# Kernel optimization log

Measured on AMD Instinct MI355X. Metric: run time of the kernel, lower is better.

Reference implementation:

```python
import jax, jax.numpy as jnp
import numpy as np

K = 20                      # kNN size (init kwarg k)
_BN_S = 1.0 / np.sqrt(1.0 + 1e-5)  # BatchNorm eval with running var=1, mean=0


def _edge_conv(f, W1, b1, g, be, W2, b2):
    # f: [B,N,C]. DynamicEdgeConv: kNN in feature space (self included, as in
    # torch_cluster.knn), message = MLP([x_i, x_j - x_i]), max aggregation.
    sq = jnp.sum(f * f, -1)
    d = sq[:, :, None] + sq[:, None, :] - 2.0 * jnp.einsum('bnc,bmc->bnm', f, f)
    _, idx = jax.lax.top_k(-d, K)                      # [B,N,K]
    fj = jax.vmap(lambda fb, ib: fb[ib])(f, idx)       # [B,N,K,C] neighbor gather
    fi = jnp.broadcast_to(f[:, :, None, :], fj.shape)
    msg = jnp.concatenate([fi, fj - fi], -1)           # [B,N,K,2C]
    h = jax.nn.relu((msg @ W1 + b1) * (g * _BN_S) + be)  # Linear -> BN(eval) -> ReLU
    h = h @ W2 + b2                                    # plain last MLP layer
    return jnp.max(h, axis=2)                          # max over K neighbors


def _forward(x, pos,
             c1_W1, c1_b1, c1_g, c1_be, c1_W2, c1_b2,
             c2_W1, c2_b1, c2_g, c2_be, c2_W2, c2_b2,
             c3_W1, c3_b1, c3_g, c3_be, c3_W2, c3_b2,
             m_W1, m_b1, m_W2, m_b2, m_W3, m_b3, m_W4, m_b4):
    x0 = jnp.concatenate([x, pos], -1)                 # [B,N,6]
    x1 = _edge_conv(x0, c1_W1, c1_b1, c1_g, c1_be, c1_W2, c1_b2)
    x2 = _edge_conv(x1, c2_W1, c2_b1, c2_g, c2_be, c2_W2, c2_b2)
    x3 = _edge_conv(x2, c3_W1, c3_b1, c3_g, c3_be, c3_W2, c3_b2)
    h = jnp.concatenate([x1, x2, x3], -1)              # [B,N,192]
    # head MLP: norm=None, dropout inactive at inference, plain last layer
    h = jax.nn.relu(h @ m_W1 + m_b1)
    h = jax.nn.relu(h @ m_W2 + m_b2)
    h = jax.nn.relu(h @ m_W3 + m_b3)
    out = h @ m_W4 + m_b4                              # [B,N,40]
    return jax.nn.log_softmax(out, -1)


def setup_inputs() -> dict:
    key = jax.random.key(0)
    ks = iter(jax.random.split(key, 40))

    def lin(cin, cout):
        W = jax.random.normal(next(ks), (cin, cout), jnp.float32) / np.sqrt(cin)
        b = jnp.zeros((cout,), jnp.float32)
        return W, b

    inp = {}
    inp['x'] = jax.random.normal(next(ks), (8, 4096, 3), jnp.float32)
    inp['pos'] = jax.random.normal(next(ks), (8, 4096, 3), jnp.float32)
    for i, cin in zip((1, 2, 3), (12, 128, 128)):      # 2*in_channels of each conv
        W1, b1 = lin(cin, 64)
        W2, b2 = lin(64, 64)
        inp[f'c{i}_W1'], inp[f'c{i}_b1'] = W1, b1
        inp[f'c{i}_g'] = jnp.ones((64,), jnp.float32)
        inp[f'c{i}_be'] = jnp.zeros((64,), jnp.float32)
        inp[f'c{i}_W2'], inp[f'c{i}_b2'] = W2, b2
    dims = [192, 1024, 256, 128, 40]
    for j in range(4):
        W, b = lin(dims[j], dims[j + 1])
        inp[f'm_W{j + 1}'], inp[f'm_b{j + 1}'] = W, b
    return inp


def reference(x, pos,
              c1_W1, c1_b1, c1_g, c1_be, c1_W2, c1_b2,
              c2_W1, c2_b1, c2_g, c2_be, c2_W2, c2_b2,
              c3_W1, c3_b1, c3_g, c3_be, c3_W2, c3_b2,
              m_W1, m_b1, m_W2, m_b2, m_W3, m_b3, m_W4, m_b4):
    return _forward(x, pos,
                    c1_W1, c1_b1, c1_g, c1_be, c1_W2, c1_b2,
                    c2_W1, c2_b1, c2_g, c2_be, c2_W2, c2_b2,
                    c3_W1, c3_b1, c3_g, c3_be, c3_W2, c3_b2,
                    m_W1, m_b1, m_W2, m_b2, m_W3, m_b3, m_W4, m_b4)
```

## Files before the change

kernel.cpp:

```cpp
#include <hip/hip_runtime.h>
#include <math.h>

#define KNN 20
#define NPTS 4096
#define NB 8

__device__ __forceinline__ bool lexless(float d1, int i1, float d2, int i2) {
    return d1 < d2 || (d1 == d2 && i1 < i2);
}

__global__ __launch_bounds__(256) void concat_norm_kernel(const float* __restrict__ x,
                                                          const float* __restrict__ pos,
                                                          float* __restrict__ f0,
                                                          float* __restrict__ nrm, int total) {
    int p = blockIdx.x * 256 + threadIdx.x;
    if (p < total) {
        float v0 = x[(size_t)p*3 + 0], v1 = x[(size_t)p*3 + 1], v2 = x[(size_t)p*3 + 2];
        float v3 = pos[(size_t)p*3 + 0], v4 = pos[(size_t)p*3 + 1], v5 = pos[(size_t)p*3 + 2];
        f0[(size_t)p*6 + 0] = v0; f0[(size_t)p*6 + 1] = v1; f0[(size_t)p*6 + 2] = v2;
        f0[(size_t)p*6 + 3] = v3; f0[(size_t)p*6 + 4] = v4; f0[(size_t)p*6 + 5] = v5;
        float s = 0.f;
        s = fmaf(v0, v0, s); s = fmaf(v1, v1, s); s = fmaf(v2, v2, s);
        s = fmaf(v3, v3, s); s = fmaf(v4, v4, s); s = fmaf(v5, v5, s);
        nrm[p] = s;
    }
}

template<int C>
__global__ __launch_bounds__(256) void norm_kernel(const float* __restrict__ f, int ldf,
                                                   float* __restrict__ norms, int total) {
    int p = blockIdx.x * 256 + threadIdx.x;
    if (p >= total) return;
    const float* fp = f + (size_t)p * ldf;
    float s = 0.f;
    if constexpr ((C & 3) == 0) {
#pragma unroll
        for (int k = 0; k < C; k += 4) {
            float4 v = *(const float4*)(fp + k);
            s = fmaf(v.x, v.x, s); s = fmaf(v.y, v.y, s);
            s = fmaf(v.z, v.z, s); s = fmaf(v.w, v.w, s);
        }
    } else {
#pragma unroll
        for (int k = 0; k < C; ++k) s = fmaf(fp[k], fp[k], s);
    }
    norms[p] = s;
}

#define KCHAIN(ck_) do {                                                 \
    unsigned long long kc = (ck_);                                       \
    _Pragma("unroll")                                                    \
    for (int t = 0; t < KNN; ++t) {                                      \
        bool sw = kc < bk[t];                                            \
        unsigned long long nn = sw ? kc : bk[t];                         \
        unsigned long long oo = sw ? bk[t] : kc;                         \
        bk[t] = nn; kc = oo;                                             \
    }                                                                    \
} while (0)

#define PACKK(dv_, jv_, out_) do {                                       \
    unsigned pu = __float_as_uint(dv_);                                  \
    pu = (pu == 0x80000000u) ? 0u : pu;                    \
    pu ^= (unsigned)((int)pu >> 31) | 0x80000000u;                       \
    (out_) = ((unsigned long long)pu << 32) | (unsigned)(jv_);           \
} while (0)

#define PUSHF(dv_, jg_) do {                                             \
    if ((dv_) <= thr) {                                                  \
        pd5 = pd4; pj5 = pj4; pd4 = pd3; pj4 = pj3;                      \
        pd3 = pd2; pj3 = pj2; pd2 = pd1; pj2 = pj1;                      \
        pd1 = pd0; pj1 = pj0; pd0 = (dv_); pj0 = (jg_); ++cnt;           \
    }                                                                    \
} while (0)

#define FLUSHF() do {                                                    \
    if (cnt > 0) { unsigned long long k0_; PACKK(pd0, pj0, k0_); KCHAIN(k0_); } \
    if (cnt > 1) { unsigned long long k1_; PACKK(pd1, pj1, k1_); KCHAIN(k1_); } \
    if (cnt > 2) { unsigned long long k2_; PACKK(pd2, pj2, k2_); KCHAIN(k2_); } \
    if (cnt > 3) { unsigned long long k3_; PACKK(pd3, pj3, k3_); KCHAIN(k3_); } \
    if (cnt > 4) { unsigned long long k4_; PACKK(pd4, pj4, k4_); KCHAIN(k4_); } \
    if (cnt > 5) { unsigned long long k5_; PACKK(pd5, pj5, k5_); KCHAIN(k5_); } \
    cnt = 0;                                                             \
    unsigned hu_ = (unsigned)(bk[KNN - 1] >> 32);                        \
    atomicMin(&thrQ[q], hu_);                                            \
    hu_ = (hu_ & 0x80000000u) ? (hu_ ^ 0x80000000u) : ~hu_;              \
    thr = __uint_as_float(hu_);                                          \
} while (0)

#define KMERGE(ptr_) do {                                                \
    const unsigned long long* mp = (ptr_);                               \
    _Pragma("unroll 1")                                                  \
    for (int tm = 0; tm < KNN; ++tm) {                                   \
        unsigned long long mk = mp[tm];                                  \
        if (mk >= bk[KNN - 1]) break;                                    \
        KCHAIN(mk);                                                      \
    }                                                                    \
} while (0)

#define KSENTINEL 0xFF800000FFFFFFFFULL

template<int C>
__global__ __launch_bounds__(128, 2) void knn_tile_kernel(const float* __restrict__ f, int ldf,
                                                          const float* __restrict__ norms,
                                                          int* __restrict__ idx) {
    const int qb    = blockIdx.x * 32;
    const int b     = qb >> 12;
    const int qloc0 = qb & (NPTS - 1);
    const int tid   = threadIdx.x;
    const int q     = tid & 31;
    const int sub   = tid >> 5;
    const int tx    = tid & 15;
    const int ty    = tid >> 4;

    union __align__(16) SM {
        struct {
            float Qs[C][32];
            float Cs[C][64];
            float Ds[32][68];
        } a;
        unsigned long long md[32][2 * KNN + 1];
    };
    __shared__ SM sm;
    __shared__ unsigned thrQ[32];

    const float* fb = f + (size_t)b * NPTS * ldf;
    const float* nb = norms + (size_t)b * NPTS;

    if (tid < 32) thrQ[tid] = 0xFFFFFFFFu;

    if constexpr ((C & 15) == 0) {
        int m = tid >> 2, ko = (tid & 3) * 4;
        const float* src = fb + (size_t)(qloc0 + m) * ldf;
#pragma unroll
        for (int k4 = ko; k4 < C; k4 += 16) {
            float4 v = *(const float4*)(src + k4);
            sm.a.Qs[k4 + 0][m] = v.x; sm.a.Qs[k4 + 1][m] = v.y;
            sm.a.Qs[k4 + 2][m] = v.z; sm.a.Qs[k4 + 3][m] = v.w;
        }
    } else {
        for (int e = tid; e < C * 32; e += 128) {
            int k = e >> 5, m = e & 31;
            sm.a.Qs[k][m] = fb[(size_t)(qloc0 + m) * ldf + k];
        }
    }

    const float4 qnv = *(const float4*)(nb + qloc0 + ty * 4);
    const float qnr[4] = {qnv.x, qnv.y, qnv.z, qnv.w};

    unsigned long long bk[KNN];
#pragma unroll
    for (int t = 0; t < KNN; ++t) bk[t] = KSENTINEL;
    float thr = INFINITY;
    float pd0 = 0.f, pd1 = 0.f, pd2 = 0.f, pd3 = 0.f, pd4 = 0.f, pd5 = 0.f;
    int   pj0 = 0, pj1 = 0, pj2 = 0, pj3 = 0, pj4 = 0, pj5 = 0;
    int   cnt = 0;

    auto stageC = [&](int j0) {
        if constexpr ((C & 7) == 0) {
            int jj = tid >> 1, ko = (tid & 1) * 4;
            const float* src = fb + (size_t)(j0 + jj) * ldf;
#pragma unroll
            for (int k4 = ko; k4 < C; k4 += 8) {
                float4 v = *(const float4*)(src + k4);
                sm.a.Cs[k4 + 0][jj] = v.x; sm.a.Cs[k4 + 1][jj] = v.y;
                sm.a.Cs[k4 + 2][jj] = v.z; sm.a.Cs[k4 + 3][jj] = v.w;
            }
        } else {
            for (int e = tid; e < C * 64; e += 128) {
                int k = e >> 6, j = e & 63;
                sm.a.Cs[k][j] = fb[(size_t)(j0 + j) * ldf + k];
            }
        }
    };

    auto gemmT = [&](int j0) {
        float acc[4][4] = {};
#pragma unroll 8
        for (int kk = 0; kk < C; ++kk) {
            float4 av = *(const float4*)&sm.a.Qs[kk][ty * 4];
            float4 bv = *(const float4*)&sm.a.Cs[kk][tx * 4];
            float a[4] = {av.x, av.y, av.z, av.w};
            float bb[4] = {bv.x, bv.y, bv.z, bv.w};
#pragma unroll
            for (int i = 0; i < 4; ++i)
#pragma unroll
                for (int j = 0; j < 4; ++j) acc[i][j] = fmaf(a[i], bb[j], acc[i][j]);
        }
        const float4 cnv = *(const float4*)(nb + j0 + tx * 4);
#pragma unroll
        for (int i = 0; i < 4; ++i) {
            float4 o;
            o.x = fmaf(-2.0f, acc[i][0], qnr[i] + cnv.x);
            o.y = fmaf(-2.0f, acc[i][1], qnr[i] + cnv.y);
            o.z = fmaf(-2.0f, acc[i][2], qnr[i] + cnv.z);
            o.w = fmaf(-2.0f, acc[i][3], qnr[i] + cnv.w);
            *(float4*)&sm.a.Ds[ty * 4 + i][tx * 4] = o;
        }
    };

    auto scanT = [&](int j0) {
        {
            unsigned su = thrQ[q];
            unsigned hu = (su & 0x80000000u) ? (su ^ 0x80000000u) : ~su;
            thr = fminf(thr, __uint_as_float(hu));
        }
        const int jb = sub * 16;
        const float4 v0 = *(const float4*)&sm.a.Ds[q][jb + 0];
        const float4 v1 = *(const float4*)&sm.a.Ds[q][jb + 4];
        const float4 v2 = *(const float4*)&sm.a.Ds[q][jb + 8];
        const float4 v3 = *(const float4*)&sm.a.Ds[q][jb + 12];
        const int jg = j0 + jb;
        PUSHF(v0.x, jg + 0);  PUSHF(v0.y, jg + 1);
        PUSHF(v0.z, jg + 2);  PUSHF(v0.w, jg + 3);  if (__any(cnt >= 3)) FLUSHF();
        PUSHF(v1.x, jg + 4);  PUSHF(v1.y, jg + 5);
        PUSHF(v1.z, jg + 6);  PUSHF(v1.w, jg + 7);  if (__any(cnt >= 3)) FLUSHF();
        PUSHF(v2.x, jg + 8);  PUSHF(v2.y, jg + 9);
        PUSHF(v2.z, jg + 10); PUSHF(v2.w, jg + 11); if (__any(cnt >= 3)) FLUSHF();
        PUSHF(v3.x, jg + 12); PUSHF(v3.y, jg + 13);
        PUSHF(v3.z, jg + 14); PUSHF(v3.w, jg + 15);
        if (__any(cnt > 0)) FLUSHF();
    };

    stageC(0);
    __syncthreads();
    gemmT(0);
    __syncthreads();
#pragma unroll 1
    for (int t = 1; t < NPTS / 64; ++t) {
        stageC(t * 64);
        scanT((t - 1) * 64);
        __syncthreads();
        gemmT(t * 64);
        __syncthreads();
    }
    scanT(NPTS - 64);
    if (__any(cnt > 0)) FLUSHF();

    __syncthreads();
    if (sub >= 2) {
#pragma unroll
        for (int t = 0; t < KNN; ++t) sm.md[q][(sub - 2) * KNN + t] = bk[t];
    }
    __syncthreads();
    if (sub < 2) KMERGE(&sm.md[q][sub * KNN]);
    __syncthreads();
    if (sub == 1) {
#pragma unroll
        for (int t = 0; t < KNN; ++t) sm.md[q][t] = bk[t];
    }
    __syncthreads();
    if (sub == 0) {
        KMERGE(&sm.md[q][0]);
        int* op = idx + (size_t)(qb + q) * KNN;
#pragma unroll
        for (int t = 0; t < KNN; ++t) op[t] = (int)bk[t];
    }
}

__global__ __launch_bounds__(128, 2) void knn6_kernel(const float* __restrict__ f,
                                                      const float* __restrict__ norms,
                                                      int* __restrict__ idx) {
    const int qb    = blockIdx.x * 32;
    const int b     = qb >> 12;
    const int qloc0 = qb & (NPTS - 1);
    const int tid   = threadIdx.x;
    const int q     = tid & 31;
    const int sub   = tid >> 5;

    __shared__ __align__(16) float Cs[2][64][8];
    __shared__ unsigned long long md[32][2 * KNN + 1];
    __shared__ unsigned thrQ[32];

    const float* fb = f + (size_t)b * NPTS * 6;
    const float* nb = norms + (size_t)b * NPTS;

    if (tid < 32) thrQ[tid] = 0xFFFFFFFFu;

    float fir[6];
    {
        const float* qsrc = fb + (size_t)(qloc0 + q) * 6;
#pragma unroll
        for (int k = 0; k < 6; ++k) fir[k] = qsrc[k];
    }
    const float qn = nb[qloc0 + q];

    unsigned long long bk[KNN];
#pragma unroll
    for (int t = 0; t < KNN; ++t) bk[t] = KSENTINEL;
    float thr = INFINITY;
    float pd0 = 0.f, pd1 = 0.f, pd2 = 0.f, pd3 = 0.f, pd4 = 0.f, pd5 = 0.f;
    int   pj0 = 0, pj1 = 0, pj2 = 0, pj3 = 0, pj4 = 0, pj5 = 0;
    int   cnt = 0;

    auto stage6 = [&](int j0, int s) {
#pragma unroll
        for (int e = tid; e < 512; e += 128) {
            int j = e >> 3, k = e & 7;
            float v = 0.f;
            if (k < 6)       v = fb[(size_t)(j0 + j) * 6 + k];
            else if (k == 6) v = nb[j0 + j];
            Cs[s][j][k] = v;
        }
    };

    auto scan6 = [&](int j0, int s) {
        {
            unsigned su = thrQ[q];
            unsigned hu = (su & 0x80000000u) ? (su ^ 0x80000000u) : ~su;
            thr = fminf(thr, __uint_as_float(hu));
        }
        const int jb = sub * 16;
#pragma unroll
        for (int jj = 0; jj < 16; ++jj) {
            const float4 c0 = *(const float4*)&Cs[s][jb + jj][0];
            const float4 c1 = *(const float4*)&Cs[s][jb + jj][4];
            float dot = 0.f;
            dot = fmaf(fir[0], c0.x, dot);
            dot = fmaf(fir[1], c0.y, dot);
            dot = fmaf(fir[2], c0.z, dot);
            dot = fmaf(fir[3], c0.w, dot);
            dot = fmaf(fir[4], c1.x, dot);
            dot = fmaf(fir[5], c1.y, dot);
            float d = fmaf(-2.0f, dot, qn + c1.z);
            PUSHF(d, j0 + jb + jj);
            if ((jj & 3) == 3) { if (__any(cnt >= 3)) FLUSHF(); }
        }
        if (__any(cnt > 0)) FLUSHF();
    };

    stage6(0, 0);
    __syncthreads();
#pragma unroll 1
    for (int t = 0; t < NPTS / 64; ++t) {
        const int cur = t & 1;
        if (t + 1 < NPTS / 64) stage6((t + 1) * 64, cur ^ 1);
        scan6(t * 64, cur);
        __syncthreads();
    }
    if (__any(cnt > 0)) FLUSHF();

    if (sub >= 2) {
#pragma unroll
        for (int t = 0; t < KNN; ++t) md[q][(sub - 2) * KNN + t] = bk[t];
    }
    __syncthreads();
    if (sub < 2) KMERGE(&md[q][sub * KNN]);
    __syncthreads();
    if (sub == 1) {
#pragma unroll
        for (int t = 0; t < KNN; ++t) md[q][t] = bk[t];
    }
    __syncthreads();
    if (sub == 0) {
        KMERGE(&md[q][0]);
        int* op = idx + (size_t)(qb + q) * KNN;
#pragma unroll
        for (int t = 0; t < KNN; ++t) op[t] = (int)bk[t];
    }
}

__global__ __launch_bounds__(256) void hg6_kernel(const float* __restrict__ f0,
                                                  const float* __restrict__ W1,
                                                  const float* __restrict__ b1,
                                                  float* __restrict__ GH, int total) {
    int t = blockIdx.x * 256 + threadIdx.x;
    if (t >= total * 128) return;
    int p  = t >> 7;
    int cc = t & 127;
    int c  = cc & 63;
    bool isG = cc >= 64;
    const float* fp = f0 + (size_t)p * 6;
    const float* Wb = W1 + (isG ? 6 * 64 : 0);
    float acc = isG ? 0.f : b1[c];
#pragma unroll
    for (int k = 0; k < 6; ++k) acc = fmaf(fp[k], Wb[k * 64 + c], acc);
    GH[(size_t)p * 128 + cc] = acc;
}

__global__ __launch_bounds__(256) void repack_w1_kernel(const float* __restrict__ W1,
                                                        const float* __restrict__ b1,
                                                        float* __restrict__ Wp,
                                                        float* __restrict__ bp) {
    int t = blockIdx.x * 256 + threadIdx.x;
    if (t < 64 * 64) {
        int k = t >> 6, c = t & 63;
        Wp[k * 128 + c]      = W1[k * 64 + c];
        Wp[k * 128 + 64 + c] = W1[(64 + k) * 64 + c];
    }
    if (t < 128) bp[t] = (t < 64) ? b1[t] : 0.f;
}

__global__ __launch_bounds__(64) void edgeconv_fact_kernel(
    const float* __restrict__ GH,
    const int* __restrict__ idx,
    const float* __restrict__ g,  const float* __restrict__ be,
    const float* __restrict__ W2, const float* __restrict__ b2,
    float* __restrict__ out, int ldo) {
    const int p = blockIdx.x;
    const int b = p >> 12;
    const int c = threadIdx.x;
    __shared__ __align__(16) float h1_s[KNN][64];
    __shared__ int nidx[KNN];
    if (c < KNN) nidx[c] = idx[(size_t)p * KNN + c];
    const float H = GH[(size_t)p * 128 + c];
    const float G = GH[(size_t)p * 128 + 64 + c];
    const float hb = H - G;
    const float bn_s = (float)(1.0 / sqrt(1.0 + 1e-5));
    const float bnscale = g[c] * bn_s;
    const float bec = be[c];
    const float* GHb = GH + (size_t)b * NPTS * 128 + 64;
    __syncthreads();
#pragma unroll
    for (int j = 0; j < KNN; ++j) {
        float gj = GHb[(size_t)nidx[j] * 128 + c];
        h1_s[j][c] = fmaxf(fmaf(hb + gj, bnscale, bec), 0.f);
    }
    __syncthreads();

    float acc2[KNN];
    float b2c = b2[c];
#pragma unroll
    for (int j = 0; j < KNN; ++j) acc2[j] = b2c;
#pragma unroll
    for (int k = 0; k < 64; k += 4) {
        float w0 = W2[(k + 0) * 64 + c];
        float w1 = W2[(k + 1) * 64 + c];
        float w2 = W2[(k + 2) * 64 + c];
        float w3 = W2[(k + 3) * 64 + c];
#pragma unroll
        for (int j = 0; j < KNN; ++j) {
            float4 v = *(const float4*)&h1_s[j][k];
            acc2[j] = fmaf(v.x, w0, acc2[j]);
            acc2[j] = fmaf(v.y, w1, acc2[j]);
            acc2[j] = fmaf(v.z, w2, acc2[j]);
            acc2[j] = fmaf(v.w, w3, acc2[j]);
        }
    }
    float m = acc2[0];
#pragma unroll
    for (int j = 1; j < KNN; ++j) m = fmaxf(m, acc2[j]);
    out[(size_t)p * ldo + c] = m;
}

template<bool RELU>
__global__ __launch_bounds__(256, 2) void gemm_kernel(
    const float* __restrict__ A, int lda,
    const float* __restrict__ W,
    const float* __restrict__ bias,
    float* __restrict__ Cc, int ldc,
    int N, int K) {
    const int BM = 128, BN = 128, BK = 16;
    __shared__ __align__(16) float As[16][128 + 4];
    __shared__ __align__(16) float Bs[16][128 + 4];
    const int bm = blockIdx.y * BM;
    const int bn = blockIdx.x * BN;
    const int tid = threadIdx.x;
    const int tx = tid & 15, ty = tid >> 4;
    float acc[8][8] = {};
    for (int k0 = 0; k0 < K; k0 += BK) {
        {
            int r = tid >> 2;
            int kq = (tid & 3) * 4;
#pragma unroll
            for (int h = 0; h < 2; ++h) {
                int rr = r + h * 64;
                float4 v = *(const float4*)(A + (size_t)(bm + rr) * lda + k0 + kq);
                As[kq + 0][rr] = v.x; As[kq + 1][rr] = v.y;
                As[kq + 2][rr] = v.z; As[kq + 3][rr] = v.w;
            }
        }
        {
            int kk = tid >> 4;
            int n8 = (tid & 15) * 8;
            float4 v0 = *(const float4*)(W + (size_t)(k0 + kk) * N + bn + n8);
            float4 v1 = *(const float4*)(W + (size_t)(k0 + kk) * N + bn + n8 + 4);
            *(float4*)&Bs[kk][n8] = v0;
            *(float4*)&Bs[kk][n8 + 4] = v1;
        }
        __syncthreads();
#pragma unroll
        for (int kk = 0; kk < BK; ++kk) {
            float4 a0 = *(const float4*)&As[kk][ty * 8];
            float4 a1 = *(const float4*)&As[kk][ty * 8 + 4];
            float4 b0 = *(const float4*)&Bs[kk][tx * 8];
            float4 b1 = *(const float4*)&Bs[kk][tx * 8 + 4];
            float a[8] = {a0.x, a0.y, a0.z, a0.w, a1.x, a1.y, a1.z, a1.w};
            float bb[8] = {b0.x, b0.y, b0.z, b0.w, b1.x, b1.y, b1.z, b1.w};
#pragma unroll
            for (int i = 0; i < 8; ++i)
#pragma unroll
                for (int j = 0; j < 8; ++j) acc[i][j] = fmaf(a[i], bb[j], acc[i][j]);
        }
        __syncthreads();
    }
    const float4 bi0 = *(const float4*)(bias + bn + tx * 8);
    const float4 bi1 = *(const float4*)(bias + bn + tx * 8 + 4);
    const float bb[8] = {bi0.x, bi0.y, bi0.z, bi0.w, bi1.x, bi1.y, bi1.z, bi1.w};
#pragma unroll
    for (int i = 0; i < 8; ++i) {
        int m = bm + ty * 8 + i;
        float4 o0, o1;
        o0.x = acc[i][0] + bb[0]; o0.y = acc[i][1] + bb[1];
        o0.z = acc[i][2] + bb[2]; o0.w = acc[i][3] + bb[3];
        o1.x = acc[i][4] + bb[4]; o1.y = acc[i][5] + bb[5];
        o1.z = acc[i][6] + bb[6]; o1.w = acc[i][7] + bb[7];
        if (RELU) {
            o0.x = fmaxf(o0.x, 0.f); o0.y = fmaxf(o0.y, 0.f);
            o0.z = fmaxf(o0.z, 0.f); o0.w = fmaxf(o0.w, 0.f);
            o1.x = fmaxf(o1.x, 0.f); o1.y = fmaxf(o1.y, 0.f);
            o1.z = fmaxf(o1.z, 0.f); o1.w = fmaxf(o1.w, 0.f);
        }
        *(float4*)(Cc + (size_t)m * ldc + bn + tx * 8) = o0;
        *(float4*)(Cc + (size_t)m * ldc + bn + tx * 8 + 4) = o1;
    }
}

__global__ __launch_bounds__(256) void head_kernel(const float* __restrict__ h3,
                                                   const float* __restrict__ W4,
                                                   const float* __restrict__ b4,
                                                   float* __restrict__ out) {
    __shared__ float W4s[128 * 40];
    __shared__ float hps[4][128];
    const int tid  = threadIdx.x;
    const int w    = tid >> 6;
    const int lane = tid & 63;
    const int p    = blockIdx.x * 4 + w;
    for (int e = tid; e < 128 * 40; e += 256) W4s[e] = W4[e];
    if (lane < 32)
        *(float4*)&hps[w][lane * 4] = *(const float4*)(h3 + (size_t)p * 128 + lane * 4);
    __syncthreads();
    float v = -INFINITY;
    if (lane < 40) {
        float acc = b4[lane];
#pragma unroll
        for (int k = 0; k < 128; ++k) acc = fmaf(hps[w][k], W4s[k * 40 + lane], acc);
        v = acc;
    }
    float mx = v;
#pragma unroll
    for (int s = 1; s < 64; s <<= 1) mx = fmaxf(mx, __shfl_xor(mx, s));
    float e = (lane < 40) ? expf(v - mx) : 0.0f;
    float se = e;
#pragma unroll
    for (int s = 1; s < 64; s <<= 1) se += __shfl_xor(se, s);
    if (lane < 40) out[(size_t)p * 40 + lane] = v - mx - logf(se);
}

extern "C" void kernel_launch(void* const* d_in, const int* in_sizes, int n_in,
                              void* d_out, int out_size, void* d_ws, size_t ws_size,
                              hipStream_t stream) {
    (void)in_sizes; (void)n_in; (void)out_size;
    const float* x     = (const float*)d_in[0];
    const float* pos   = (const float*)d_in[1];
    const float* c1_W1 = (const float*)d_in[2];
    const float* c1_b1 = (const float*)d_in[3];
    const float* c1_g  = (const float*)d_in[4];
    const float* c1_be = (const float*)d_in[5];
    const float* c1_W2 = (const float*)d_in[6];
    const float* c1_b2 = (const float*)d_in[7];
    const float* c2_W1 = (const float*)d_in[8];
    const float* c2_b1 = (const float*)d_in[9];
    const float* c2_g  = (const float*)d_in[10];
    const float* c2_be = (const float*)d_in[11];
    const float* c2_W2 = (const float*)d_in[12];
    const float* c2_b2 = (const float*)d_in[13];
    const float* c3_W1 = (const float*)d_in[14];
    const float* c3_b1 = (const float*)d_in[15];
    const float* c3_g  = (const float*)d_in[16];
    const float* c3_be = (const float*)d_in[17];
    const float* c3_W2 = (const float*)d_in[18];
    const float* c3_b2 = (const float*)d_in[19];
    const float* m_W1  = (const float*)d_in[20];
    const float* m_b1  = (const float*)d_in[21];
    const float* m_W2  = (const float*)d_in[22];
    const float* m_b2  = (const float*)d_in[23];
    const float* m_W3  = (const float*)d_in[24];
    const float* m_b3  = (const float*)d_in[25];
    const float* m_W4  = (const float*)d_in[26];
    const float* m_b4  = (const float*)d_in[27];
    float* out = (float*)d_out;

    const int TOT = NB * NPTS;

    float* ws   = (float*)d_ws;
    float* f0   = ws;
    int*   idxb = (int*)(ws + 196608);
    float* feat = ws + 196608 + 655360;

    const size_t basef  = 196608 + 655360 + 6291456;
    const size_t availf = ws_size / 4;
    int MC = 4096;
    if (availf >= basef + (size_t)32768 * 1408) MC = 32768;
    else if (availf >= basef + (size_t)16384 * 1408) MC = 16384;
    else if (availf >= basef + (size_t)8192 * 1408) MC = 8192;

    float* h1   = feat + 6291456;
    float* h2   = h1 + (size_t)MC * 1024;
    float* h3   = h2 + (size_t)MC * 256;
    float* nrm  = h1;
    float* GH   = h1 + 131072;
    float* Wp   = GH + (size_t)TOT * 128;
    float* bp   = Wp + 8192;

    concat_norm_kernel<<<(TOT + 255) / 256, 256, 0, stream>>>(x, pos, f0, nrm, TOT);
    knn6_kernel<<<TOT / 32, 128, 0, stream>>>(f0, nrm, idxb);
    hg6_kernel<<<(TOT * 128) / 256, 256, 0, stream>>>(f0, c1_W1, c1_b1, GH, TOT);
    edgeconv_fact_kernel<<<TOT, 64, 0, stream>>>(GH, idxb,
        c1_g, c1_be, c1_W2, c1_b2, feat + 0, 192);

    norm_kernel<64><<<(TOT + 255) / 256, 256, 0, stream>>>(feat + 0, 192, nrm, TOT);
    knn_tile_kernel<64><<<TOT / 32, 128, 0, stream>>>(feat + 0, 192, nrm, idxb);
    repack_w1_kernel<<<16, 256, 0, stream>>>(c2_W1, c2_b1, Wp, bp);
    gemm_kernel<false><<<dim3(1, TOT / 128), 256, 0, stream>>>(
        feat + 0, 192, Wp, bp, GH, 128, 128, 64);
    edgeconv_fact_kernel<<<TOT, 64, 0, stream>>>(GH, idxb,
        c2_g, c2_be, c2_W2, c2_b2, feat + 64, 192);

    norm_kernel<64><<<(TOT + 255) / 256, 256, 0, stream>>>(feat + 64, 192, nrm, TOT);
    knn_tile_kernel<64><<<TOT / 32, 128, 0, stream>>>(feat + 64, 192, nrm, idxb);
    repack_w1_kernel<<<16, 256, 0, stream>>>(c3_W1, c3_b1, Wp, bp);
    gemm_kernel<false><<<dim3(1, TOT / 128), 256, 0, stream>>>(
        feat + 64, 192, Wp, bp, GH, 128, 128, 64);
    edgeconv_fact_kernel<<<TOT, 64, 0, stream>>>(GH, idxb,
        c3_g, c3_be, c3_W2, c3_b2, feat + 128, 192);

    for (int mc = 0; mc < TOT; mc += MC) {
        gemm_kernel<true><<<dim3(1024 / 128, MC / 128), 256, 0, stream>>>(
            feat + (size_t)mc * 192, 192, m_W1, m_b1, h1, 1024, 1024, 192);
        gemm_kernel<true><<<dim3(256 / 128, MC / 128), 256, 0, stream>>>(
            h1, 1024, m_W2, m_b2, h2, 256, 256, 1024);
        gemm_kernel<true><<<dim3(128 / 128, MC / 128), 256, 0, stream>>>(
            h2, 256, m_W3, m_b3, h3, 128, 128, 256);
        head_kernel<<<MC / 4, 256, 0, stream>>>(h3, m_W4, m_b4, out + (size_t)mc * 40);
    }
}
```

Baseline: 2.134 ms.

## Double-buffer GEMM shared tiles with register prefetch and drop redundant kNN flushes

The head-MLP GEMM kernel now uses two shared-memory buffers and prefetches the next K-slice into registers while computing on the current one. This halves the barriers per iteration and hides global-load latency behind the FMAs. The kNN scan loops also drop the unconditional end-of-tile flush and only flush when a lane's candidate buffer nears capacity, relying on the final flush after the loop. The cost is double the shared memory and more registers in the GEMM, which could lower occupancy.

```diff
diff --git a/kernel.cpp b/kernel.cpp
--- a/kernel.cpp
+++ b/kernel.cpp
@@ -217,8 +217,7 @@
         PUSHF(v2.x, jg + 8);  PUSHF(v2.y, jg + 9);
         PUSHF(v2.z, jg + 10); PUSHF(v2.w, jg + 11); if (__any(cnt >= 3)) FLUSHF();
         PUSHF(v3.x, jg + 12); PUSHF(v3.y, jg + 13);
-        PUSHF(v3.z, jg + 14); PUSHF(v3.w, jg + 15);
-        if (__any(cnt > 0)) FLUSHF();
+        PUSHF(v3.z, jg + 14); PUSHF(v3.w, jg + 15); if (__any(cnt >= 3)) FLUSHF();
     };
 
     stageC(0);
@@ -325,7 +324,6 @@
             PUSHF(d, j0 + jb + jj);
             if ((jj & 3) == 3) { if (__any(cnt >= 3)) FLUSHF(); }
         }
-        if (__any(cnt > 0)) FLUSHF();
     };
 
     stage6(0, 0);
@@ -449,47 +447,62 @@
     const float* __restrict__ bias,
     float* __restrict__ Cc, int ldc,
     int N, int K) {
-    const int BM = 128, BN = 128, BK = 16;
-    __shared__ __align__(16) float As[16][128 + 4];
-    __shared__ __align__(16) float Bs[16][128 + 4];
-    const int bm = blockIdx.y * BM;
-    const int bn = blockIdx.x * BN;
+    __shared__ __align__(16) float As[2][16][128 + 4];
+    __shared__ __align__(16) float Bs[2][16][128 + 4];
+    const int bm = blockIdx.y * 128;
+    const int bn = blockIdx.x * 128;
     const int tid = threadIdx.x;
     const int tx = tid & 15, ty = tid >> 4;
+    const int r  = tid >> 2, kq = (tid & 3) * 4;
+    const int kw = tid >> 4, n8 = (tid & 15) * 8;
+    const int nk = K / 16;
     float acc[8][8] = {};
-    for (int k0 = 0; k0 < K; k0 += BK) {
-        {
-            int r = tid >> 2;
-            int kq = (tid & 3) * 4;
-#pragma unroll
-            for (int h = 0; h < 2; ++h) {
-                int rr = r + h * 64;
-                float4 v = *(const float4*)(A + (size_t)(bm + rr) * lda + k0 + kq);
-                As[kq + 0][rr] = v.x; As[kq + 1][rr] = v.y;
-                As[kq + 2][rr] = v.z; As[kq + 3][rr] = v.w;
-            }
-        }
-        {
-            int kk = tid >> 4;
-            int n8 = (tid & 15) * 8;
-            float4 v0 = *(const float4*)(W + (size_t)(k0 + kk) * N + bn + n8);
-            float4 v1 = *(const float4*)(W + (size_t)(k0 + kk) * N + bn + n8 + 4);
-            *(float4*)&Bs[kk][n8] = v0;
-            *(float4*)&Bs[kk][n8 + 4] = v1;
-        }
-        __syncthreads();
-#pragma unroll
-        for (int kk = 0; kk < BK; ++kk) {
-            float4 a0 = *(const float4*)&As[kk][ty * 8];
-            float4 a1 = *(const float4*)&As[kk][ty * 8 + 4];
-            float4 b0 = *(const float4*)&Bs[kk][tx * 8];
-            float4 b1 = *(const float4*)&Bs[kk][tx * 8 + 4];
+    {
+        float4 a0 = *(const float4*)(A + (size_t)(bm + r) * lda + kq);
+        float4 a1 = *(const float4*)(A + (size_t)(bm + r + 64) * lda + kq);
+        As[0][kq + 0][r] = a0.x; As[0][kq + 1][r] = a0.y;
+        As[0][kq + 2][r] = a0.z; As[0][kq + 3][r] = a0.w;
+        As[0][kq + 0][r + 64] = a1.x; As[0][kq + 1][r + 64] = a1.y;
+        As[0][kq + 2][r + 64] = a1.z; As[0][kq + 3][r + 64] = a1.w;
+        float4 w0 = *(const float4*)(W + (size_t)kw * N + bn + n8);
+        float4 w1 = *(const float4*)(W + (size_t)kw * N + bn + n8 + 4);
+        *(float4*)&Bs[0][kw][n8] = w0;
+        *(float4*)&Bs[0][kw][n8 + 4] = w1;
+    }
+    __syncthreads();
+#pragma unroll 1
+    for (int t = 0; t < nk; ++t) {
+        const int cur = t & 1;
+        float4 pa0, pa1, pw0, pw1;
+        const bool more = (t + 1 < nk);
+        if (more) {
+            int k0 = (t + 1) * 16;
+            pa0 = *(const float4*)(A + (size_t)(bm + r) * lda + k0 + kq);
+            pa1 = *(const float4*)(A + (size_t)(bm + r + 64) * lda + k0 + kq);
+            pw0 = *(const float4*)(W + (size_t)(k0 + kw) * N + bn + n8);
+            pw1 = *(const float4*)(W + (size_t)(k0 + kw) * N + bn + n8 + 4);
+        }
+#pragma unroll
+        for (int kk = 0; kk < 16; ++kk) {
+            float4 a0 = *(const float4*)&As[cur][kk][ty * 8];
+            float4 a1 = *(const float4*)&As[cur][kk][ty * 8 + 4];
+            float4 b0 = *(const float4*)&Bs[cur][kk][tx * 8];
+            float4 b1 = *(const float4*)&Bs[cur][kk][tx * 8 + 4];
             float a[8] = {a0.x, a0.y, a0.z, a0.w, a1.x, a1.y, a1.z, a1.w};
             float bb[8] = {b0.x, b0.y, b0.z, b0.w, b1.x, b1.y, b1.z, b1.w};
 #pragma unroll
             for (int i = 0; i < 8; ++i)
 #pragma unroll
                 for (int j = 0; j < 8; ++j) acc[i][j] = fmaf(a[i], bb[j], acc[i][j]);
+        }
+        if (more) {
+            const int nxt = cur ^ 1;
+            As[nxt][kq + 0][r] = pa0.x; As[nxt][kq + 1][r] = pa0.y;
+            As[nxt][kq + 2][r] = pa0.z; As[nxt][kq + 3][r] = pa0.w;
+            As[nxt][kq + 0][r + 64] = pa1.x; As[nxt][kq + 1][r + 64] = pa1.y;
+            As[nxt][kq + 2][r + 64] = pa1.z; As[nxt][kq + 3][r + 64] = pa1.w;
+            *(float4*)&Bs[nxt][kw][n8] = pw0;
+            *(float4*)&Bs[nxt][kw][n8 + 4] = pw1;
         }
         __syncthreads();
     }
```

Result: slower. 4.125 ms (+93.3%).
